# Performance work log

Hardware: AMD Instinct MI355X
Metric: run time of the kernel (lower is better)

## Reference

```python
import jax, jax.numpy as jnp
import numpy as np

NUM_SUBJECTS = 2048
NUM_TRIALS = 40  # -> num_paths = C(43,3) = 12341
NUM_STATES = 4


def _enumerate_paths(num_trials):
    # All monotone non-decreasing state sequences over {0,1,2,3}, same order
    # as the torch cached_property `paths`.
    paths = [[0], [1], [2], [3]]
    for _ in range(num_trials - 1):
        paths = [p + [s] for p in paths for s in range(p[-1], NUM_STATES)]
    return np.asarray(paths, dtype=np.int32)  # [P, T]


def setup_inputs() -> dict:
    key = jax.random.key(0)
    k1, k2, k3, k4 = jax.random.split(key, 4)
    return {
        "subject_responses": jax.random.randint(
            k1, (NUM_SUBJECTS, NUM_TRIALS), 0, NUM_STATES, dtype=jnp.int32),
        "paths": jnp.asarray(_enumerate_paths(NUM_TRIALS)),
        "w_strategy_success": jax.random.uniform(k2, (4, 4), dtype=jnp.float32),
        "w_state_priors": jax.random.uniform(k3, (4,), dtype=jnp.float32),
        "w_transitions": jax.random.uniform(k4, (4, 4), dtype=jnp.float32),
    }


def reference(subject_responses, paths, w_strategy_success, w_state_priors,
              w_transitions):
    # Fixed constants from the module
    strat_mask = jnp.triu(jnp.full((4, 4), -jnp.inf, dtype=jnp.float32), k=1)
    trans_mask = jnp.tril(jnp.full((4, 4), -jnp.inf, dtype=jnp.float32), k=-1)
    p_strategy_responses = jnp.array(
        [[3 / 9, 4 / 9, 1 / 9, 1 / 9],
         [0.0, 4 / 6, 1 / 6, 1 / 6],
         [0.0, 0.0, 0.5, 0.5],
         [0.0, 0.0, 0.0, 1.0]], dtype=jnp.float32)

    # Parameter transforms
    p_strategy_success = jax.nn.softmax(w_strategy_success + strat_mask, axis=-1)
    p_state_responses = p_strategy_success @ p_strategy_responses        # [4,4]
    p_state_priors = jax.nn.softmax(w_state_priors)                      # [4]
    p_transitions = jax.nn.softmax(w_transitions + trans_mask, axis=-1)  # [4,4]

    # P(path): log prior of first state + sum of log transition probs
    log_tr = jnp.log(p_transitions)
    log_p_paths = (jnp.log(p_state_priors)[paths[:, 0]]
                   + log_tr[paths[:, :-1], paths[:, 1:]].sum(-1))  # [P]
    p_paths = jnp.exp(log_p_paths)

    # P(responses | path) per subject: sum_t log p_state_responses[state_t, resp_t]
    # expressed as a dense contraction (P, T*4) x (T*4, S) for efficiency.
    log_sr = jnp.log(p_state_responses)                  # [state, response]
    paths_oh = jax.nn.one_hot(paths, NUM_STATES, dtype=log_sr.dtype)  # [P,T,4]
    resp_log = log_sr.T[subject_responses]               # [S,T,4]; [s,t,k]=log_sr[k, r_st]
    log_lik = jnp.einsum('ptk,stk->sp', paths_oh, resp_log)  # [S,P]
    likelihoods = jnp.exp(log_lik)

    # P(path | responses)
    numerator = p_paths[None, :] * likelihoods           # [S,P]
    posteriors = numerator / numerator.sum(-1, keepdims=True)
    return posteriors
```

## Files before the change

### kernel.cpp

```cpp
#include <hip/hip_runtime.h>
#include <math.h>

#define NSUB   2048
#define NTRIAL 40
#define NPATH  12341
#define NITER  ((NPATH + 255) / 256)

__global__ void param_kernel(const float* __restrict__ w_ss,
                             const float* __restrict__ w_sp,
                             const float* __restrict__ w_tr,
                             float* __restrict__ params) {
    if (threadIdx.x != 0 || blockIdx.x != 0) return;
    const float psr[4][4] = {
        {3.f/9.f, 4.f/9.f, 1.f/9.f, 1.f/9.f},
        {0.f,     4.f/6.f, 1.f/6.f, 1.f/6.f},
        {0.f,     0.f,     0.5f,    0.5f},
        {0.f,     0.f,     0.f,     1.f}};
    float pss[4][4];
    for (int i = 0; i < 4; i++) {
        float m = -1e30f;
        for (int j = 0; j <= i; j++) m = fmaxf(m, w_ss[i*4+j]);
        float e[4] = {0.f,0.f,0.f,0.f}, s = 0.f;
        for (int j = 0; j <= i; j++) { e[j] = __expf(w_ss[i*4+j] - m); s += e[j]; }
        for (int j = 0; j < 4; j++) pss[i][j] = (j <= i) ? e[j]/s : 0.f;
    }
    for (int i = 0; i < 4; i++)
        for (int r = 0; r < 4; r++) {
            float acc = 0.f;
            for (int j = 0; j < 4; j++) acc += pss[i][j] * psr[j][r];
            params[i*4+r] = logf(acc);
        }
    {
        float m = fmaxf(fmaxf(w_sp[0], w_sp[1]), fmaxf(w_sp[2], w_sp[3]));
        float e[4], s = 0.f;
        for (int k = 0; k < 4; k++) { e[k] = __expf(w_sp[k] - m); s += e[k]; }
        for (int k = 0; k < 4; k++) params[16+k] = logf(e[k]/s);
    }
    for (int i = 0; i < 4; i++) {
        float m = -1e30f;
        for (int j = i; j < 4; j++) m = fmaxf(m, w_tr[i*4+j]);
        float e[4] = {0.f,0.f,0.f,0.f}, s = 0.f;
        for (int j = i; j < 4; j++) { e[j] = __expf(w_tr[i*4+j] - m); s += e[j]; }
        for (int j = 0; j < 4; j++)
            params[20+i*4+j] = (j >= i) ? logf(e[j]/s) : -1e30f;
    }
}

__global__ void path_kernel(const int* __restrict__ paths,
                            const float* __restrict__ params,
                            float* __restrict__ logp,
                            int* __restrict__ bp) {
    int p = blockIdx.x * blockDim.x + threadIdx.x;
    if (p >= NPATH) return;
    const int* pp = paths + (size_t)p * NTRIAL;
    int s0 = pp[0];
    float lp = params[16 + s0];
    int c0 = (s0 == 0), c1 = (s0 <= 1), c2 = (s0 <= 2);
    int prev = s0;
    for (int t = 1; t < NTRIAL; t++) {
        int st = pp[t];
        lp += params[20 + prev*4 + st];
        c0 += (st == 0); c1 += (st <= 1); c2 += (st <= 2);
        prev = st;
    }
    logp[p] = lp;
    bp[p] = c0 | (c1 << 6) | (c2 << 12);
}

__global__ __launch_bounds__(256) void post_kernel(
        const int* __restrict__ resp,
        const float* __restrict__ params,
        const float* __restrict__ logp,
        const int* __restrict__ bp,
        float* __restrict__ out) {
    __shared__ float C[4][44];
    __shared__ int   rs[NTRIAL];
    __shared__ float red[4];
    __shared__ float s_inv;

    const int s = blockIdx.x;
    const int tid = threadIdx.x;

    if (tid < NTRIAL) rs[tid] = resp[(size_t)s * NTRIAL + tid];
    __syncthreads();
    if (tid < 4) {
        float c = 0.f;
        C[tid][0] = 0.f;
        for (int t = 0; t < NTRIAL; t++) {
            c += params[tid*4 + rs[t]];
            C[tid][t+1] = c;
        }
    }
    __syncthreads();
    const float CT3 = C[3][NTRIAL];

    float nums[NITER];
    float lsum = 0.f;
#pragma unroll
    for (int i = 0; i < NITER; i++) {
        int p = tid + 256 * i;
        float v = 0.f;
        if (p < NPATH) {
            int b  = bp[p];
            int t1 = b & 63, t2 = (b >> 6) & 63, t3 = (b >> 12) & 63;
            float ll = C[0][t1] + (C[1][t2] - C[1][t1])
                     + (C[2][t3] - C[2][t2]) + (CT3 - C[3][t3]);
            v = __expf(logp[p] + ll);
        }
        nums[i] = v;
        lsum += v;
    }

    for (int off = 32; off > 0; off >>= 1)
        lsum += __shfl_down(lsum, off, 64);
    const int wave = tid >> 6, lane = tid & 63;
    if (lane == 0) red[wave] = lsum;
    __syncthreads();
    if (tid == 0) s_inv = 1.f / (red[0] + red[1] + red[2] + red[3]);
    __syncthreads();
    const float inv = s_inv;

    float* orow = out + (size_t)s * NPATH;
#pragma unroll
    for (int i = 0; i < NITER; i++) {
        int p = tid + 256 * i;
        if (p < NPATH) orow[p] = nums[i] * inv;
    }
}

extern "C" void kernel_launch(void* const* d_in, const int* in_sizes, int n_in,
                              void* d_out, int out_size, void* d_ws, size_t ws_size,
                              hipStream_t stream) {
    const int*   resp  = (const int*)d_in[0];
    const int*   paths = (const int*)d_in[1];
    const float* w_ss  = (const float*)d_in[2];
    const float* w_sp  = (const float*)d_in[3];
    const float* w_tr  = (const float*)d_in[4];
    float* out = (float*)d_out;

    float* params = (float*)d_ws;
    float* logp   = params + 64;
    int*   bp     = (int*)(params + 64 + 12352);

    param_kernel<<<1, 64, 0, stream>>>(w_ss, w_sp, w_tr, params);
    path_kernel<<<(NPATH + 255) / 256, 256, 0, stream>>>(paths, params, logp, bp);
    post_kernel<<<NSUB, 256, 0, stream>>>(resp, params, logp, bp, out);
}
```

Before: 167.4 us.

## Fold parameter kernel into path and posterior kernels, widen posterior blocks

Removes the single-thread parameter kernel: the prior and transition log-softmax are now computed per block inside the path kernel, and the state-response log table is computed inside the posterior kernel. Path log-probability and the packed count word are written together as one int2 record, path rows are read with int4 vector loads, and the likelihood uses precomputed prefix-difference tables. The posterior kernel moves from 256 to 1024 threads per block. This drops one launch and some serial work, but each block now recomputes the small parameter tables redundantly, and larger blocks may change occupancy.

```diff
diff --git a/kernel.cpp b/kernel.cpp
--- a/kernel.cpp
+++ b/kernel.cpp
@@ -4,108 +4,115 @@
 #define NSUB   2048
 #define NTRIAL 40
 #define NPATH  12341
-#define NITER  ((NPATH + 255) / 256)
+#define PBLK   1024
+#define NIT    ((NPATH + PBLK - 1) / PBLK)
 
-__global__ void param_kernel(const float* __restrict__ w_ss,
-                             const float* __restrict__ w_sp,
-                             const float* __restrict__ w_tr,
-                             float* __restrict__ params) {
-    if (threadIdx.x != 0 || blockIdx.x != 0) return;
-    const float psr[4][4] = {
-        {3.f/9.f, 4.f/9.f, 1.f/9.f, 1.f/9.f},
-        {0.f,     4.f/6.f, 1.f/6.f, 1.f/6.f},
-        {0.f,     0.f,     0.5f,    0.5f},
-        {0.f,     0.f,     0.f,     1.f}};
-    float pss[4][4];
-    for (int i = 0; i < 4; i++) {
+__global__ __launch_bounds__(256) void path_kernel(
+        const int* __restrict__ paths,
+        const float* __restrict__ w_sp,
+        const float* __restrict__ w_tr,
+        int2* __restrict__ rec) {
+    __shared__ float sprior[4];
+    __shared__ float str[16];
+    const int tid = threadIdx.x;
+
+    if (tid < 4) {
+        float m = fmaxf(fmaxf(w_sp[0], w_sp[1]), fmaxf(w_sp[2], w_sp[3]));
+        float s = 0.f;
+        for (int k = 0; k < 4; k++) s += __expf(w_sp[k] - m);
+        sprior[tid] = w_sp[tid] - (__logf(s) + m);
+    } else if (tid < 20) {
+        int idx = tid - 4, i = idx >> 2, j = idx & 3;
         float m = -1e30f;
-        for (int j = 0; j <= i; j++) m = fmaxf(m, w_ss[i*4+j]);
-        float e[4] = {0.f,0.f,0.f,0.f}, s = 0.f;
-        for (int j = 0; j <= i; j++) { e[j] = __expf(w_ss[i*4+j] - m); s += e[j]; }
-        for (int j = 0; j < 4; j++) pss[i][j] = (j <= i) ? e[j]/s : 0.f;
+        for (int k = i; k < 4; k++) m = fmaxf(m, w_tr[i*4 + k]);
+        float s = 0.f;
+        for (int k = i; k < 4; k++) s += __expf(w_tr[i*4 + k] - m);
+        str[idx] = (j >= i) ? (w_tr[i*4 + j] - (__logf(s) + m)) : 0.f;
     }
-    for (int i = 0; i < 4; i++)
-        for (int r = 0; r < 4; r++) {
-            float acc = 0.f;
-            for (int j = 0; j < 4; j++) acc += pss[i][j] * psr[j][r];
-            params[i*4+r] = logf(acc);
-        }
-    {
-        float m = fmaxf(fmaxf(w_sp[0], w_sp[1]), fmaxf(w_sp[2], w_sp[3]));
-        float e[4], s = 0.f;
-        for (int k = 0; k < 4; k++) { e[k] = __expf(w_sp[k] - m); s += e[k]; }
-        for (int k = 0; k < 4; k++) params[16+k] = logf(e[k]/s);
+    __syncthreads();
+
+    int p = blockIdx.x * 256 + tid;
+    if (p >= NPATH) return;
+
+    const int4* pp = (const int4*)(paths + (size_t)p * NTRIAL);
+    int st[NTRIAL];
+#pragma unroll
+    for (int q = 0; q < NTRIAL / 4; q++) {
+        int4 v = pp[q];
+        st[4*q] = v.x; st[4*q+1] = v.y; st[4*q+2] = v.z; st[4*q+3] = v.w;
     }
-    for (int i = 0; i < 4; i++) {
-        float m = -1e30f;
-        for (int j = i; j < 4; j++) m = fmaxf(m, w_tr[i*4+j]);
-        float e[4] = {0.f,0.f,0.f,0.f}, s = 0.f;
-        for (int j = i; j < 4; j++) { e[j] = __expf(w_tr[i*4+j] - m); s += e[j]; }
-        for (int j = 0; j < 4; j++)
-            params[20+i*4+j] = (j >= i) ? logf(e[j]/s) : -1e30f;
+    float lp = sprior[st[0]];
+    int c0 = (st[0] == 0), c1 = (st[0] <= 1), c2 = (st[0] <= 2);
+#pragma unroll
+    for (int t = 1; t < NTRIAL; t++) {
+        lp += str[st[t-1]*4 + st[t]];
+        c0 += (st[t] == 0); c1 += (st[t] <= 1); c2 += (st[t] <= 2);
     }
+    rec[p] = make_int2(__float_as_int(lp), c0 | (c1 << 6) | (c2 << 12));
 }
 
-__global__ void path_kernel(const int* __restrict__ paths,
-                            const float* __restrict__ params,
-                            float* __restrict__ logp,
-                            int* __restrict__ bp) {
-    int p = blockIdx.x * blockDim.x + threadIdx.x;
-    if (p >= NPATH) return;
-    const int* pp = paths + (size_t)p * NTRIAL;
-    int s0 = pp[0];
-    float lp = params[16 + s0];
-    int c0 = (s0 == 0), c1 = (s0 <= 1), c2 = (s0 <= 2);
-    int prev = s0;
-    for (int t = 1; t < NTRIAL; t++) {
-        int st = pp[t];
-        lp += params[20 + prev*4 + st];
-        c0 += (st == 0); c1 += (st <= 1); c2 += (st <= 2);
-        prev = st;
-    }
-    logp[p] = lp;
-    bp[p] = c0 | (c1 << 6) | (c2 << 12);
-}
-
-__global__ __launch_bounds__(256) void post_kernel(
+__global__ __launch_bounds__(1024) void post_kernel(
         const int* __restrict__ resp,
-        const float* __restrict__ params,
-        const float* __restrict__ logp,
-        const int* __restrict__ bp,
+        const float* __restrict__ w_ss,
+        const int2* __restrict__ rec,
         float* __restrict__ out) {
-    __shared__ float C[4][44];
+    __shared__ float lsr[16];
     __shared__ int   rs[NTRIAL];
-    __shared__ float red[4];
-    __shared__ float s_inv;
+    __shared__ float C[4][NTRIAL + 1];
+    __shared__ float D1[NTRIAL + 1], D2[NTRIAL + 1], D3[NTRIAL + 1];
+    __shared__ float red[16];
+    __shared__ float bcast[2];
 
     const int s = blockIdx.x;
     const int tid = threadIdx.x;
 
+    if (tid < 16) {
+        const float psr[4][4] = {
+            {3.f/9.f, 4.f/9.f, 1.f/9.f, 1.f/9.f},
+            {0.f,     4.f/6.f, 1.f/6.f, 1.f/6.f},
+            {0.f,     0.f,     0.5f,    0.5f},
+            {0.f,     0.f,     0.f,     1.f}};
+        int i = tid >> 2, r = tid & 3;
+        float m = -1e30f;
+        for (int j = 0; j <= i; j++) m = fmaxf(m, w_ss[i*4 + j]);
+        float e[4] = {0.f,0.f,0.f,0.f}, ssum = 0.f;
+        for (int j = 0; j <= i; j++) { e[j] = __expf(w_ss[i*4 + j] - m); ssum += e[j]; }
+        float acc = 0.f;
+        for (int j = 0; j <= i; j++) acc += (e[j] / ssum) * psr[j][r];
+        lsr[tid] = __logf(acc);
+    }
     if (tid < NTRIAL) rs[tid] = resp[(size_t)s * NTRIAL + tid];
     __syncthreads();
+
     if (tid < 4) {
         float c = 0.f;
         C[tid][0] = 0.f;
         for (int t = 0; t < NTRIAL; t++) {
-            c += params[tid*4 + rs[t]];
+            c += lsr[tid*4 + rs[t]];
             C[tid][t+1] = c;
         }
     }
     __syncthreads();
-    const float CT3 = C[3][NTRIAL];
+    if (tid <= NTRIAL) {
+        D1[tid] = C[0][tid] - C[1][tid];
+        D2[tid] = C[1][tid] - C[2][tid];
+        D3[tid] = C[2][tid] - C[3][tid];
+    }
+    if (tid == 0) bcast[0] = C[3][NTRIAL];
+    __syncthreads();
+    const float CT3 = bcast[0];
 
-    float nums[NITER];
+    float nums[NIT];
     float lsum = 0.f;
 #pragma unroll
-    for (int i = 0; i < NITER; i++) {
-        int p = tid + 256 * i;
+    for (int i = 0; i < NIT; i++) {
+        int p = tid + PBLK * i;
         float v = 0.f;
         if (p < NPATH) {
-            int b  = bp[p];
+            int2 r2 = rec[p];
+            int b = r2.y;
             int t1 = b & 63, t2 = (b >> 6) & 63, t3 = (b >> 12) & 63;
-            float ll = C[0][t1] + (C[1][t2] - C[1][t1])
-                     + (C[2][t3] - C[2][t2]) + (CT3 - C[3][t3]);
-            v = __expf(logp[p] + ll);
+            v = __expf(__int_as_float(r2.x) + D1[t1] + D2[t2] + D3[t3] + CT3);
         }
         nums[i] = v;
         lsum += v;
@@ -116,14 +123,18 @@
     const int wave = tid >> 6, lane = tid & 63;
     if (lane == 0) red[wave] = lsum;
     __syncthreads();
-    if (tid == 0) s_inv = 1.f / (red[0] + red[1] + red[2] + red[3]);
+    if (tid == 0) {
+        float t = 0.f;
+        for (int w = 0; w < 16; w++) t += red[w];
+        bcast[1] = 1.f / t;
+    }
     __syncthreads();
-    const float inv = s_inv;
+    const float inv = bcast[1];
 
     float* orow = out + (size_t)s * NPATH;
 #pragma unroll
-    for (int i = 0; i < NITER; i++) {
-        int p = tid + 256 * i;
+    for (int i = 0; i < NIT; i++) {
+        int p = tid + PBLK * i;
         if (p < NPATH) orow[p] = nums[i] * inv;
     }
 }
@@ -138,11 +149,8 @@
     const float* w_tr  = (const float*)d_in[4];
     float* out = (float*)d_out;
 
-    float* params = (float*)d_ws;
-    float* logp   = params + 64;
-    int*   bp     = (int*)(params + 64 + 12352);
+    int2* rec = (int2*)d_ws;
 
-    param_kernel<<<1, 64, 0, stream>>>(w_ss, w_sp, w_tr, params);
-    path_kernel<<<(NPATH + 255) / 256, 256, 0, stream>>>(paths, params, logp, bp);
-    post_kernel<<<NSUB, 256, 0, stream>>>(resp, params, logp, bp, out);
+    path_kernel<<<(NPATH + 255) / 256, 256, 0, stream>>>(paths, w_sp, w_tr, rec);
+    post_kernel<<<NSUB, PBLK, 0, stream>>>(resp, w_ss, rec, out);
 }
```

Measured after the change: 147.2 us. 12.1% less time.
